# Optimization experiments

Measured on AMD Instinct MI355X. Metric: run time of the kernel, lower is better.

Reference implementation:

```python
import jax, jax.numpy as jnp
import numpy as np

N_NODES = 50000
N_EDGES = 800000
IN_CH, HID_CH, OUT_CH = 128, 128, 64


def _glorot(key, out_c, in_c):
    lim = (6.0 / (in_c + out_c)) ** 0.5
    return jax.random.uniform(key, (out_c, in_c), jnp.float32, -lim, lim)


def setup_inputs() -> dict:
    key = jax.random.key(0)
    ks = jax.random.split(key, 12)
    x = jax.random.normal(ks[0], (N_NODES, IN_CH), jnp.float32)
    edge_index = jax.random.randint(ks[1], (2, N_EDGES), 0, N_NODES, dtype=jnp.int64)
    # 4 SAGEConv layers: 128->128, 128->128, 128->64, 64->64
    dims = [(IN_CH, HID_CH), (HID_CH, HID_CH), (HID_CH, OUT_CH), (OUT_CH, OUT_CH)]
    params = {}
    for i, (ci, co) in enumerate(dims, start=1):
        params[f"Wl{i}"] = _glorot(ks[2 * i], co, ci)          # neighbor (aggregated) transform
        params[f"bl{i}"] = jnp.zeros((co,), jnp.float32)
        params[f"Wr{i}"] = _glorot(ks[2 * i + 1], co, ci)      # root/self transform (no bias in PyG)
    return {"x": x, "edge_index": edge_index, **params}


def _sage_conv(x, src, dst, Wl, bl, Wr):
    # mean aggregation of source features at destination nodes
    msgs = x[src]                                                   # [E, C] gather
    summed = jax.ops.segment_sum(msgs, dst, num_segments=N_NODES)   # [N, C] scatter-add
    cnt = jax.ops.segment_sum(jnp.ones((src.shape[0], 1), x.dtype), dst, num_segments=N_NODES)
    mean = summed / jnp.maximum(cnt, 1.0)
    return mean @ Wl.T + bl + x @ Wr.T


def reference(x, edge_index, Wl1, bl1, Wr1, Wl2, bl2, Wr2, Wl3, bl3, Wr3, Wl4, bl4, Wr4):
    src, dst = edge_index[0], edge_index[1]
    # conv1 = GraphSAGE(in, hid, num_layers=2): relu between layers only
    h = jax.nn.relu(_sage_conv(x, src, dst, Wl1, bl1, Wr1))
    h = _sage_conv(h, src, dst, Wl2, bl2, Wr2)
    h = jax.nn.relu(h)  # model-level .relu()
    # conv2 = GraphSAGE(hid, out, num_layers=2)
    h = jax.nn.relu(_sage_conv(h, src, dst, Wl3, bl3, Wr3))
    h = _sage_conv(h, src, dst, Wl4, bl4, Wr4)
    return jax.nn.log_softmax(h, axis=1)
```

## Files before the change

kernel.cpp:

```cpp
#include <hip/hip_runtime.h>
#include <hip/hip_bf16.h>


typedef __attribute__((ext_vector_type(8))) short bf16x8;
typedef __attribute__((ext_vector_type(4))) float f32x4;

#define NB 128
#define BSHIFT 9
#define BCAP 12288
#define EPB 2048

__device__ __forceinline__ unsigned short f2bf(float f) {
    __hip_bfloat16 h = __float2bfloat16(f);
    return __builtin_bit_cast(unsigned short, h);
}
__device__ __forceinline__ float bflo(unsigned int u) {
    return __builtin_bit_cast(float, u << 16);
}
__device__ __forceinline__ float bfhi(unsigned int u) {
    return __builtin_bit_cast(float, u & 0xffff0000u);
}

__global__ __launch_bounds__(256) void f2bf_bulk(const float* __restrict__ in,
                                                 unsigned short* __restrict__ out,
                                                 int n4) {
    int i = blockIdx.x * 256 + threadIdx.x;
    if (i < n4) {
        float4 v = reinterpret_cast<const float4*>(in)[i];
        ushort4 o = {f2bf(v.x), f2bf(v.y), f2bf(v.z), f2bf(v.w)};
        reinterpret_cast<ushort4*>(out)[i] = o;
    }
}

__global__ void zero_ints(int* __restrict__ p, int n) {
    int i = blockIdx.x * blockDim.x + threadIdx.x;
    if (i < n) p[i] = 0;
}

__global__ __launch_bounds__(256) void partition_edges(
    const int* __restrict__ ei, int E,
    int* __restrict__ gcur, unsigned int* __restrict__ ppk)
{
    __shared__ int hist[NB];
    __shared__ int base[NB];
    const int tid = threadIdx.x;
    for (int i = tid; i < NB; i += 256) hist[i] = 0;
    __syncthreads();

    const int e0 = blockIdx.x * EPB;
    int bket[8], rank[8];
    unsigned int pk[8];
    #pragma unroll
    for (int k = 0; k < 8; ++k) {
        int e = e0 + k * 256 + tid;
        bket[k] = -1;
        if (e < E) {
            int d = ei[E + e], s = ei[e];
            int b = d >> BSHIFT;
            bket[k] = b;
            pk[k] = ((unsigned int)(d - (b << BSHIFT)) << 16) | (unsigned int)s;
            rank[k] = atomicAdd(&hist[b], 1);
        }
    }
    __syncthreads();
    for (int i = tid; i < NB; i += 256)
        base[i] = hist[i] ? atomicAdd(&gcur[i], hist[i]) : 0;
    __syncthreads();
    #pragma unroll
    for (int k = 0; k < 8; ++k) {
        if (bket[k] >= 0) {
            int off = base[bket[k]] + rank[k];
            if (off < BCAP)
                ppk[(size_t)bket[k] * BCAP + off] = pk[k];
        }
    }
}

__global__ __launch_bounds__(256) void count_part(
    const unsigned int* __restrict__ ppk, const int* __restrict__ gcur,
    int* __restrict__ cnt)
{
    const int b = blockIdx.y;
    const int n = min(gcur[b], BCAP);
    const int tid = threadIdx.x;
    #pragma unroll
    for (int k = 0; k < 8; ++k) {
        int idx = blockIdx.x * EPB + k * 256 + tid;
        if (idx < n) {
            unsigned int pk = ppk[(size_t)b * BCAP + idx];
            atomicAdd(&cnt[(b << BSHIFT) + (int)(pk >> 16)], 1);
        }
    }
}

__global__ void block_sums(const int* __restrict__ cnt, int* __restrict__ bsum, int N) {
    int i = blockIdx.x * 256 + threadIdx.x;
    int v = (i < N) ? cnt[i] : 0;
    #pragma unroll
    for (int off = 32; off; off >>= 1) v += __shfl_down(v, off);
    __shared__ int ws_[4];
    int lane = threadIdx.x & 63, wid = threadIdx.x >> 6;
    if (lane == 0) ws_[wid] = v;
    __syncthreads();
    if (threadIdx.x == 0) bsum[blockIdx.x] = ws_[0] + ws_[1] + ws_[2] + ws_[3];
}

__global__ void scan_bsums(int* __restrict__ bsum, int nb) {
    int tid = threadIdx.x;
    int v = (tid < nb) ? bsum[tid] : 0;
    int lane = tid & 63, wid = tid >> 6;
    int x = v;
    #pragma unroll
    for (int d = 1; d < 64; d <<= 1) {
        int t = __shfl_up(x, d);
        if (lane >= d) x += t;
    }
    __shared__ int wsum[4];
    if (lane == 63) wsum[wid] = x;
    __syncthreads();
    int add = 0;
    for (int w = 0; w < wid; ++w) add += wsum[w];
    int incl = x + add;
    if (tid < nb) bsum[tid] = incl - v;
}

__global__ void scan_final(const int* __restrict__ cnt, const int* __restrict__ bsum,
                           int* __restrict__ offs, int* __restrict__ cursor, int N) {
    int b = blockIdx.x, tid = threadIdx.x;
    int i = b * 256 + tid;
    int v = (i < N) ? cnt[i] : 0;
    int lane = tid & 63, wid = tid >> 6;
    int x = v;
    #pragma unroll
    for (int d = 1; d < 64; d <<= 1) {
        int t = __shfl_up(x, d);
        if (lane >= d) x += t;
    }
    __shared__ int wsum[4];
    if (lane == 63) wsum[wid] = x;
    __syncthreads();
    int add = bsum[b];
    for (int w = 0; w < wid; ++w) add += wsum[w];
    int excl = add + x - v;
    if (i < N) { offs[i] = excl; cursor[i] = excl; }
    if (i == N - 1) offs[N] = excl + v;
}

__global__ __launch_bounds__(256) void fill_part(
    const unsigned int* __restrict__ ppk, const int* __restrict__ gcur,
    int* __restrict__ cursor, int* __restrict__ srcs)
{
    const int b = blockIdx.y;
    const int n = min(gcur[b], BCAP);
    const int tid = threadIdx.x;
    #pragma unroll
    for (int k = 0; k < 8; ++k) {
        int idx = blockIdx.x * EPB + k * 256 + tid;
        if (idx < n) {
            unsigned int pk = ppk[(size_t)b * BCAP + idx];
            int d = (b << BSHIFT) + (int)(pk >> 16);
            int slot = atomicAdd(&cursor[d], 1);
            srcs[slot] = (int)(pk & 0xffffu);
        }
    }
}

template <int K, int Cout, int ZBF>
__global__ __launch_bounds__(256) void gemm_yz_mfma(
    const unsigned short* __restrict__ H,
    const float* __restrict__ Wl, const float* __restrict__ Wr,
    unsigned short* __restrict__ Y, unsigned short* __restrict__ Zb,
    float* __restrict__ Zf, int N)
{
    constexpr int BM = 128, BN = 128;
    constexpr int ROWH = K + 8;
    __shared__ unsigned short Hs[BM * ROWH];
    __shared__ unsigned short Ws[BN * ROWH];

    const int tid = threadIdx.x;
    const int bm = blockIdx.x * BM;
    const int bn = blockIdx.y * BN;

    constexpr int C8 = K / 8;
    constexpr int NCH = BM * C8;
    #pragma unroll
    for (int c = tid; c < NCH; c += 256) {
        int row = c / C8, k8 = (c % C8) * 8;
        int grow = bm + row;
        int4 v = {0, 0, 0, 0};
        if (grow < N) v = *reinterpret_cast<const int4*>(&H[(size_t)grow * K + k8]);
        *reinterpret_cast<int4*>(&Hs[row * ROWH + k8]) = v;
    }
    constexpr int C4 = K / 4;
    constexpr int NCW = BN * C4;
    #pragma unroll
    for (int c = tid; c < NCW; c += 256) {
        int row = c / C4, k4 = (c % C4) * 4;
        int gcol = bn + row;
        const float* wsrc = (gcol < Cout) ? (Wl + (size_t)gcol * K)
                                          : (Wr + (size_t)(gcol - Cout) * K);
        float4 v = *reinterpret_cast<const float4*>(wsrc + k4);
        ushort4 o = {f2bf(v.x), f2bf(v.y), f2bf(v.z), f2bf(v.w)};
        *reinterpret_cast<ushort4*>(&Ws[row * ROWH + k4]) = o;
    }
    __syncthreads();

    const int wid = tid >> 6, lane = tid & 63;
    const int wr = wid >> 1, wc = wid & 1;
    const int l15 = lane & 15, lhi = lane >> 4;

    f32x4 acc[4][4] = {};
    #pragma unroll
    for (int k0 = 0; k0 < K; k0 += 32) {
        const int colOff = k0 + lhi * 8;
        bf16x8 a[4], b[4];
        #pragma unroll
        for (int m = 0; m < 4; ++m)
            a[m] = *reinterpret_cast<const bf16x8*>(&Hs[(wr * 64 + m * 16 + l15) * ROWH + colOff]);
        #pragma unroll
        for (int n = 0; n < 4; ++n)
            b[n] = *reinterpret_cast<const bf16x8*>(&Ws[(wc * 64 + n * 16 + l15) * ROWH + colOff]);
        #pragma unroll
        for (int m = 0; m < 4; ++m)
            #pragma unroll
            for (int n = 0; n < 4; ++n)
                acc[m][n] = __builtin_amdgcn_mfma_f32_16x16x32_bf16(a[m], b[n], acc[m][n], 0, 0, 0);
    }

    #pragma unroll
    for (int m = 0; m < 4; ++m) {
        #pragma unroll
        for (int n = 0; n < 4; ++n) {
            int gcol = bn + wc * 64 + n * 16 + l15;
            #pragma unroll
            for (int j = 0; j < 4; ++j) {
                int grow = bm + wr * 64 + m * 16 + lhi * 4 + j;
                if (grow < N) {
                    if (gcol < Cout)      Y[(size_t)grow * Cout + gcol] = f2bf(acc[m][n][j]);
                    else if (ZBF)         Zb[(size_t)grow * Cout + (gcol - Cout)] = f2bf(acc[m][n][j]);
                    else                  Zf[(size_t)grow * Cout + (gcol - Cout)] = acc[m][n][j];
                }
            }
        }
    }
}

__global__ __launch_bounds__(64) void agg128_bf(
    const unsigned short* __restrict__ Y, const unsigned short* __restrict__ Zb,
    const float* __restrict__ bl,
    const int* __restrict__ offs, const int* __restrict__ srcs,
    unsigned short* __restrict__ OUT)
{
    const int node = blockIdx.x;
    const int lane = threadIdx.x;
    const int beg = offs[node], end = offs[node + 1];

    float a0 = 0.f, a1 = 0.f;
    int e = beg;
    for (; e + 4 <= end; e += 4) {
        int s0 = srcs[e], s1 = srcs[e + 1], s2 = srcs[e + 2], s3 = srcs[e + 3];
        unsigned int u0 = *reinterpret_cast<const unsigned int*>(&Y[(size_t)s0 * 128 + 2 * lane]);
        unsigned int u1 = *reinterpret_cast<const unsigned int*>(&Y[(size_t)s1 * 128 + 2 * lane]);
        unsigned int u2 = *reinterpret_cast<const unsigned int*>(&Y[(size_t)s2 * 128 + 2 * lane]);
        unsigned int u3 = *reinterpret_cast<const unsigned int*>(&Y[(size_t)s3 * 128 + 2 * lane]);
        a0 += bflo(u0) + bflo(u1) + bflo(u2) + bflo(u3);
        a1 += bfhi(u0) + bfhi(u1) + bfhi(u2) + bfhi(u3);
    }
    for (; e < end; ++e) {
        unsigned int u = *reinterpret_cast<const unsigned int*>(&Y[(size_t)srcs[e] * 128 + 2 * lane]);
        a0 += bflo(u); a1 += bfhi(u);
    }
    float inv = 1.0f / fmaxf((float)(end - beg), 1.0f);
    unsigned int zu = *reinterpret_cast<const unsigned int*>(&Zb[(size_t)node * 128 + 2 * lane]);
    float2 bb = *reinterpret_cast<const float2*>(&bl[2 * lane]);
    float o0 = fmaxf(a0 * inv + bflo(zu) + bb.x, 0.f);
    float o1 = fmaxf(a1 * inv + bfhi(zu) + bb.y, 0.f);
    unsigned int packed = (unsigned int)f2bf(o0) | ((unsigned int)f2bf(o1) << 16);
    *reinterpret_cast<unsigned int*>(&OUT[(size_t)node * 128 + 2 * lane]) = packed;
}

template <int RELU, int BF16OUT, int ZBF>
__global__ __launch_bounds__(64) void agg64_k(
    const unsigned short* __restrict__ Y,
    const unsigned short* __restrict__ Zb, const float* __restrict__ Zf,
    const float* __restrict__ bl,
    const int* __restrict__ offs, const int* __restrict__ srcs,
    unsigned short* __restrict__ OUTb, float* __restrict__ OUTf)
{
    const int node = blockIdx.x;
    const int lane = threadIdx.x;
    const int half = lane >> 5, l31 = lane & 31;
    const int beg = offs[node], end = offs[node + 1];

    float a0 = 0.f, a1 = 0.f;
    int e = beg + half;
    for (; e + 2 < end; e += 4) {
        int s0 = srcs[e], s1 = srcs[e + 2];
        unsigned int u0 = *reinterpret_cast<const unsigned int*>(&Y[(size_t)s0 * 64 + 2 * l31]);
        unsigned int u1 = *reinterpret_cast<const unsigned int*>(&Y[(size_t)s1 * 64 + 2 * l31]);
        a0 += bflo(u0) + bflo(u1);
        a1 += bfhi(u0) + bfhi(u1);
    }
    if (e < end) {
        unsigned int u = *reinterpret_cast<const unsigned int*>(&Y[(size_t)srcs[e] * 64 + 2 * l31]);
        a0 += bflo(u); a1 += bfhi(u);
    }
    a0 += __shfl_xor(a0, 32);
    a1 += __shfl_xor(a1, 32);

    if (lane < 32) {
        float inv = 1.0f / fmaxf((float)(end - beg), 1.0f);
        float z0, z1;
        if (ZBF) {
            unsigned int zu = *reinterpret_cast<const unsigned int*>(&Zb[(size_t)node * 64 + 2 * l31]);
            z0 = bflo(zu); z1 = bfhi(zu);
        } else {
            float2 z = *reinterpret_cast<const float2*>(&Zf[(size_t)node * 64 + 2 * l31]);
            z0 = z.x; z1 = z.y;
        }
        float2 bb = *reinterpret_cast<const float2*>(&bl[2 * l31]);
        float o0 = a0 * inv + z0 + bb.x;
        float o1 = a1 * inv + z1 + bb.y;
        if (RELU) { o0 = fmaxf(o0, 0.f); o1 = fmaxf(o1, 0.f); }
        if (BF16OUT) {
            unsigned int packed = (unsigned int)f2bf(o0) | ((unsigned int)f2bf(o1) << 16);
            *reinterpret_cast<unsigned int*>(&OUTb[(size_t)node * 64 + 2 * l31]) = packed;
        } else {
            *reinterpret_cast<float2*>(&OUTf[(size_t)node * 64 + 2 * l31]) = make_float2(o0, o1);
        }
    }
}

__global__ __launch_bounds__(64) void logsoftmax64(
    const float* __restrict__ in, float* __restrict__ out, int N)
{
    const int r = blockIdx.x;
    const int lane = threadIdx.x;
    float v = in[(size_t)r * 64 + lane];
    float m = v;
    #pragma unroll
    for (int off = 32; off; off >>= 1) m = fmaxf(m, __shfl_xor(m, off));
    float e = expf(v - m);
    float s = e;
    #pragma unroll
    for (int off = 32; off; off >>= 1) s += __shfl_xor(s, off);
    out[(size_t)r * 64 + lane] = (v - m) - logf(s);
}

extern "C" void kernel_launch(void* const* d_in, const int* in_sizes, int n_in,
                              void* d_out, int out_size, void* d_ws, size_t ws_size,
                              hipStream_t stream) {
    const float* x   = (const float*)d_in[0];
    const int*   ei  = (const int*)d_in[1];
    const float* Wl1 = (const float*)d_in[2];
    const float* bl1 = (const float*)d_in[3];
    const float* Wr1 = (const float*)d_in[4];
    const float* Wl2 = (const float*)d_in[5];
    const float* bl2 = (const float*)d_in[6];
    const float* Wr2 = (const float*)d_in[7];
    const float* Wl3 = (const float*)d_in[8];
    const float* bl3 = (const float*)d_in[9];
    const float* Wr3 = (const float*)d_in[10];
    const float* Wl4 = (const float*)d_in[11];
    const float* bl4 = (const float*)d_in[12];
    const float* Wr4 = (const float*)d_in[13];

    const int N = in_sizes[0] / 128;
    const int E = in_sizes[1] / 2;

    char* p = (char*)d_ws;
    auto alloc = [&](size_t bytes) {
        char* r = p;
        p += (bytes + 255) & ~(size_t)255;
        return r;
    };
    int*            cnt    = (int*)alloc((size_t)N * 4);
    int*            offs   = (int*)alloc((size_t)(N + 1) * 4);
    int*            cursor = (int*)alloc((size_t)N * 4);
    int*            bsum   = (int*)alloc(256 * 4);
    int*            gcur   = (int*)alloc(NB * 4);
    unsigned int*   ppk    = (unsigned int*)alloc((size_t)NB * BCAP * 4);
    int*            srcs   = (int*)alloc((size_t)E * 4);
    unsigned short* xb     = (unsigned short*)alloc((size_t)N * 128 * 2);
    unsigned short* ybuf   = (unsigned short*)alloc((size_t)N * 128 * 2);
    char*           zraw   = alloc((size_t)N * 128 * 4);
    unsigned short* h1     = (unsigned short*)alloc((size_t)N * 128 * 2);
    unsigned short* h2     = (unsigned short*)alloc((size_t)N * 128 * 2);
    unsigned short* h3     = (unsigned short*)alloc((size_t)N * 64 * 2);
    float*          hf     = (float*)alloc((size_t)N * 64 * 4);
    unsigned short* zb     = (unsigned short*)zraw;
    float*          zf     = (float*)zraw;
    (void)ws_size; (void)n_in; (void)out_size;

    const int nb = (N + 255) / 256;
    const int mtiles = (N + 127) / 128;

    f2bf_bulk<<<(N * 128 / 4 + 255) / 256, 256, 0, stream>>>(x, xb, N * 128 / 4);

    zero_ints<<<(N + 255) / 256, 256, 0, stream>>>(cnt, N);
    zero_ints<<<1, NB, 0, stream>>>(gcur, NB);
    partition_edges<<<(E + EPB - 1) / EPB, 256, 0, stream>>>(ei, E, gcur, ppk);
    count_part<<<dim3(BCAP / EPB, NB), 256, 0, stream>>>(ppk, gcur, cnt);
    block_sums<<<nb, 256, 0, stream>>>(cnt, bsum, N);
    scan_bsums<<<1, 256, 0, stream>>>(bsum, nb);
    scan_final<<<nb, 256, 0, stream>>>(cnt, bsum, offs, cursor, N);
    fill_part<<<dim3(BCAP / EPB, NB), 256, 0, stream>>>(ppk, gcur, cursor, srcs);

    gemm_yz_mfma<128, 128, 1><<<dim3(mtiles, 2), 256, 0, stream>>>(xb, Wl1, Wr1, ybuf, zb, nullptr, N);
    agg128_bf<<<N, 64, 0, stream>>>(ybuf, zb, bl1, offs, srcs, h1);
    gemm_yz_mfma<128, 128, 1><<<dim3(mtiles, 2), 256, 0, stream>>>(h1, Wl2, Wr2, ybuf, zb, nullptr, N);
    agg128_bf<<<N, 64, 0, stream>>>(ybuf, zb, bl2, offs, srcs, h2);
    gemm_yz_mfma<128, 64, 1><<<dim3(mtiles, 1), 256, 0, stream>>>(h2, Wl3, Wr3, ybuf, zb, nullptr, N);
    agg64_k<1, 1, 1><<<N, 64, 0, stream>>>(ybuf, zb, nullptr, bl3, offs, srcs, h3, nullptr);
    gemm_yz_mfma<64, 64, 0><<<dim3(mtiles, 1), 256, 0, stream>>>(h3, Wl4, Wr4, ybuf, nullptr, zf, N);
    agg64_k<0, 0, 0><<<N, 64, 0, stream>>>(ybuf, nullptr, zf, bl4, offs, srcs, nullptr, hf);

    logsoftmax64<<<N, 64, 0, stream>>>(hf, (float*)d_out, N);
}
```

Before: 374.7 us.

## Replace CSR build with per-bucket LDS sort and fuse conversion and log-softmax

The multi-kernel CSR build (count, three-stage scan, fill with global atomics) is replaced by finer 512-bucket partitioning, a single-block scan of bucket totals, and a per-bucket shared-memory counting sort that writes srcs and offs directly. The standalone fp32-to-bf16 conversion of x is folded into the first GEMM's tile load, and log-softmax is fused into the last aggregation kernel. Aggregation kernels now pack four nodes per 256-thread block. This cuts kernel launches, global atomics and intermediate buffers. It relies on every bucket holding at most 3072 edges and on per-bucket ordering being consistent.

```diff
diff --git a/kernel.cpp b/kernel.cpp
--- a/kernel.cpp
+++ b/kernel.cpp
@@ -5,9 +5,9 @@
 typedef __attribute__((ext_vector_type(8))) short bf16x8;
 typedef __attribute__((ext_vector_type(4))) float f32x4;
 
-#define NB 128
-#define BSHIFT 9
-#define BCAP 12288
+#define NBKT 512
+#define BSHIFT 7
+#define BCAP 3072
 #define EPB 2048
 
 __device__ __forceinline__ unsigned short f2bf(float f) {
@@ -21,17 +21,6 @@
     return __builtin_bit_cast(float, u & 0xffff0000u);
 }
 
-__global__ __launch_bounds__(256) void f2bf_bulk(const float* __restrict__ in,
-                                                 unsigned short* __restrict__ out,
-                                                 int n4) {
-    int i = blockIdx.x * 256 + threadIdx.x;
-    if (i < n4) {
-        float4 v = reinterpret_cast<const float4*>(in)[i];
-        ushort4 o = {f2bf(v.x), f2bf(v.y), f2bf(v.z), f2bf(v.w)};
-        reinterpret_cast<ushort4*>(out)[i] = o;
-    }
-}
-
 __global__ void zero_ints(int* __restrict__ p, int n) {
     int i = blockIdx.x * blockDim.x + threadIdx.x;
     if (i < n) p[i] = 0;
@@ -41,10 +30,10 @@
     const int* __restrict__ ei, int E,
     int* __restrict__ gcur, unsigned int* __restrict__ ppk)
 {
-    __shared__ int hist[NB];
-    __shared__ int base[NB];
+    __shared__ int hist[NBKT];
+    __shared__ int base[NBKT];
     const int tid = threadIdx.x;
-    for (int i = tid; i < NB; i += 256) hist[i] = 0;
+    for (int i = tid; i < NBKT; i += 256) hist[i] = 0;
     __syncthreads();
 
     const int e0 = blockIdx.x * EPB;
@@ -58,12 +47,12 @@
             int d = ei[E + e], s = ei[e];
             int b = d >> BSHIFT;
             bket[k] = b;
-            pk[k] = ((unsigned int)(d - (b << BSHIFT)) << 16) | (unsigned int)s;
+            pk[k] = ((unsigned int)(d & ((1 << BSHIFT) - 1)) << 16) | (unsigned int)s;
             rank[k] = atomicAdd(&hist[b], 1);
         }
     }
     __syncthreads();
-    for (int i = tid; i < NB; i += 256)
+    for (int i = tid; i < NBKT; i += 256)
         base[i] = hist[i] ? atomicAdd(&gcur[i], hist[i]) : 0;
     __syncthreads();
     #pragma unroll
@@ -76,98 +65,82 @@
     }
 }
 
-__global__ __launch_bounds__(256) void count_part(
-    const unsigned int* __restrict__ ppk, const int* __restrict__ gcur,
-    int* __restrict__ cnt)
-{
-    const int b = blockIdx.y;
-    const int n = min(gcur[b], BCAP);
+__global__ __launch_bounds__(512) void scan_gcur(
+    const int* __restrict__ gcur, int* __restrict__ bbase,
+    int* __restrict__ offs, int N)
+{
     const int tid = threadIdx.x;
-    #pragma unroll
-    for (int k = 0; k < 8; ++k) {
-        int idx = blockIdx.x * EPB + k * 256 + tid;
-        if (idx < n) {
-            unsigned int pk = ppk[(size_t)b * BCAP + idx];
-            atomicAdd(&cnt[(b << BSHIFT) + (int)(pk >> 16)], 1);
-        }
-    }
-}
-
-__global__ void block_sums(const int* __restrict__ cnt, int* __restrict__ bsum, int N) {
-    int i = blockIdx.x * 256 + threadIdx.x;
-    int v = (i < N) ? cnt[i] : 0;
-    #pragma unroll
-    for (int off = 32; off; off >>= 1) v += __shfl_down(v, off);
-    __shared__ int ws_[4];
-    int lane = threadIdx.x & 63, wid = threadIdx.x >> 6;
-    if (lane == 0) ws_[wid] = v;
-    __syncthreads();
-    if (threadIdx.x == 0) bsum[blockIdx.x] = ws_[0] + ws_[1] + ws_[2] + ws_[3];
-}
-
-__global__ void scan_bsums(int* __restrict__ bsum, int nb) {
-    int tid = threadIdx.x;
-    int v = (tid < nb) ? bsum[tid] : 0;
-    int lane = tid & 63, wid = tid >> 6;
+    int v = min(gcur[tid], BCAP);
     int x = v;
     #pragma unroll
     for (int d = 1; d < 64; d <<= 1) {
         int t = __shfl_up(x, d);
-        if (lane >= d) x += t;
-    }
-    __shared__ int wsum[4];
-    if (lane == 63) wsum[wid] = x;
+        if ((tid & 63) >= d) x += t;
+    }
+    __shared__ int ws[8];
+    if ((tid & 63) == 63) ws[tid >> 6] = x;
     __syncthreads();
     int add = 0;
-    for (int w = 0; w < wid; ++w) add += wsum[w];
+    for (int w = 0; w < (tid >> 6); ++w) add += ws[w];
     int incl = x + add;
-    if (tid < nb) bsum[tid] = incl - v;
-}
-
-__global__ void scan_final(const int* __restrict__ cnt, const int* __restrict__ bsum,
-                           int* __restrict__ offs, int* __restrict__ cursor, int N) {
-    int b = blockIdx.x, tid = threadIdx.x;
-    int i = b * 256 + tid;
-    int v = (i < N) ? cnt[i] : 0;
-    int lane = tid & 63, wid = tid >> 6;
-    int x = v;
-    #pragma unroll
-    for (int d = 1; d < 64; d <<= 1) {
-        int t = __shfl_up(x, d);
-        if (lane >= d) x += t;
-    }
-    __shared__ int wsum[4];
-    if (lane == 63) wsum[wid] = x;
-    __syncthreads();
-    int add = bsum[b];
-    for (int w = 0; w < wid; ++w) add += wsum[w];
-    int excl = add + x - v;
-    if (i < N) { offs[i] = excl; cursor[i] = excl; }
-    if (i == N - 1) offs[N] = excl + v;
-}
-
-__global__ __launch_bounds__(256) void fill_part(
+    bbase[tid] = incl - v;
+    if (tid == 511) offs[N] = incl;
+}
+
+__global__ __launch_bounds__(256) void bucket_sort(
     const unsigned int* __restrict__ ppk, const int* __restrict__ gcur,
-    int* __restrict__ cursor, int* __restrict__ srcs)
-{
-    const int b = blockIdx.y;
+    const int* __restrict__ bbase,
+    int* __restrict__ offs, int* __restrict__ srcs, int N)
+{
+    const int b = blockIdx.x;
     const int n = min(gcur[b], BCAP);
+    const int bb = bbase[b];
     const int tid = threadIdx.x;
-    #pragma unroll
-    for (int k = 0; k < 8; ++k) {
-        int idx = blockIdx.x * EPB + k * 256 + tid;
-        if (idx < n) {
-            unsigned int pk = ppk[(size_t)b * BCAP + idx];
-            int d = (b << BSHIFT) + (int)(pk >> 16);
-            int slot = atomicAdd(&cursor[d], 1);
-            srcs[slot] = (int)(pk & 0xffffu);
-        }
-    }
-}
-
-template <int K, int Cout, int ZBF>
+
+    __shared__ unsigned int eL[BCAP];
+    __shared__ int cnt[1 << BSHIFT], excl[1 << BSHIFT], cur[1 << BSHIFT];
+
+    if (tid < (1 << BSHIFT)) cnt[tid] = 0;
+    for (int i = tid; i < n; i += 256) eL[i] = ppk[(size_t)b * BCAP + i];
+    __syncthreads();
+    for (int i = tid; i < n; i += 256) atomicAdd(&cnt[eL[i] >> 16], 1);
+    __syncthreads();
+
+    int v = 0, x = 0;
+    if (tid < 128) {
+        v = cnt[tid];
+        x = v;
+        #pragma unroll
+        for (int d = 1; d < 64; d <<= 1) {
+            int t = __shfl_up(x, d);
+            if ((tid & 63) >= d) x += t;
+        }
+    }
+    __shared__ int w0;
+    if (tid == 63) w0 = x;
+    __syncthreads();
+    if (tid < 128) {
+        int incl = x + ((tid >= 64) ? w0 : 0);
+        excl[tid] = incl - v;
+        cur[tid] = incl - v;
+    }
+    __syncthreads();
+
+    for (int i = tid; i < n; i += 256) {
+        unsigned int pk = eL[i];
+        int d = (int)(pk >> 16);
+        int pos = atomicAdd(&cur[d], 1);
+        srcs[bb + pos] = (int)(pk & 0xffffu);
+    }
+    if (tid < 128) {
+        int gn = (b << BSHIFT) + tid;
+        if (gn < N) offs[gn] = bb + excl[tid];
+    }
+}
+
+template <int K, int Cout, int ZBF, int F32IN>
 __global__ __launch_bounds__(256) void gemm_yz_mfma(
-    const unsigned short* __restrict__ H,
+    const void* __restrict__ Hv,
     const float* __restrict__ Wl, const float* __restrict__ Wr,
     unsigned short* __restrict__ Y, unsigned short* __restrict__ Zb,
     float* __restrict__ Zf, int N)
@@ -181,27 +154,39 @@
     const int bm = blockIdx.x * BM;
     const int bn = blockIdx.y * BN;
 
-    constexpr int C8 = K / 8;
-    constexpr int NCH = BM * C8;
-    #pragma unroll
-    for (int c = tid; c < NCH; c += 256) {
-        int row = c / C8, k8 = (c % C8) * 8;
-        int grow = bm + row;
-        int4 v = {0, 0, 0, 0};
-        if (grow < N) v = *reinterpret_cast<const int4*>(&H[(size_t)grow * K + k8]);
-        *reinterpret_cast<int4*>(&Hs[row * ROWH + k8]) = v;
-    }
-    constexpr int C4 = K / 4;
-    constexpr int NCW = BN * C4;
-    #pragma unroll
-    for (int c = tid; c < NCW; c += 256) {
-        int row = c / C4, k4 = (c % C4) * 4;
-        int gcol = bn + row;
-        const float* wsrc = (gcol < Cout) ? (Wl + (size_t)gcol * K)
-                                          : (Wr + (size_t)(gcol - Cout) * K);
-        float4 v = *reinterpret_cast<const float4*>(wsrc + k4);
-        ushort4 o = {f2bf(v.x), f2bf(v.y), f2bf(v.z), f2bf(v.w)};
-        *reinterpret_cast<ushort4*>(&Ws[row * ROWH + k4]) = o;
+    if (F32IN) {
+        const float* H = (const float*)Hv;
+        constexpr int C4 = K / 4;
+        for (int c = tid; c < BM * C4; c += 256) {
+            int row = c / C4, k4 = (c % C4) * 4;
+            int grow = bm + row;
+            float4 vv = make_float4(0.f, 0.f, 0.f, 0.f);
+            if (grow < N) vv = *reinterpret_cast<const float4*>(&H[(size_t)grow * K + k4]);
+            ushort4 o = {f2bf(vv.x), f2bf(vv.y), f2bf(vv.z), f2bf(vv.w)};
+            *reinterpret_cast<ushort4*>(&Hs[row * ROWH + k4]) = o;
+        }
+    } else {
+        const unsigned short* H = (const unsigned short*)Hv;
+        constexpr int C8 = K / 8;
+        for (int c = tid; c < BM * C8; c += 256) {
+            int row = c / C8, k8 = (c % C8) * 8;
+            int grow = bm + row;
+            int4 vv = {0, 0, 0, 0};
+            if (grow < N) vv = *reinterpret_cast<const int4*>(&H[(size_t)grow * K + k8]);
+            *reinterpret_cast<int4*>(&Hs[row * ROWH + k8]) = vv;
+        }
+    }
+    {
+        constexpr int C4 = K / 4;
+        for (int c = tid; c < BN * C4; c += 256) {
+            int row = c / C4, k4 = (c % C4) * 4;
+            int gcol = bn + row;
+            const float* wsrc = (gcol < Cout) ? (Wl + (size_t)gcol * K)
+                                              : (Wr + (size_t)(gcol - Cout) * K);
+            float4 vv = *reinterpret_cast<const float4*>(wsrc + k4);
+            ushort4 o = {f2bf(vv.x), f2bf(vv.y), f2bf(vv.z), f2bf(vv.w)};
+            *reinterpret_cast<ushort4*>(&Ws[row * ROWH + k4]) = o;
+        }
     }
     __syncthreads();
 
@@ -213,46 +198,47 @@
     #pragma unroll
     for (int k0 = 0; k0 < K; k0 += 32) {
         const int colOff = k0 + lhi * 8;
-        bf16x8 a[4], b[4];
+        bf16x8 a[4], bfr[4];
         #pragma unroll
         for (int m = 0; m < 4; ++m)
             a[m] = *reinterpret_cast<const bf16x8*>(&Hs[(wr * 64 + m * 16 + l15) * ROWH + colOff]);
         #pragma unroll
-        for (int n = 0; n < 4; ++n)
-            b[n] = *reinterpret_cast<const bf16x8*>(&Ws[(wc * 64 + n * 16 + l15) * ROWH + colOff]);
+        for (int nn = 0; nn < 4; ++nn)
+            bfr[nn] = *reinterpret_cast<const bf16x8*>(&Ws[(wc * 64 + nn * 16 + l15) * ROWH + colOff]);
         #pragma unroll
         for (int m = 0; m < 4; ++m)
             #pragma unroll
-            for (int n = 0; n < 4; ++n)
-                acc[m][n] = __builtin_amdgcn_mfma_f32_16x16x32_bf16(a[m], b[n], acc[m][n], 0, 0, 0);
+            for (int nn = 0; nn < 4; ++nn)
+                acc[m][nn] = __builtin_amdgcn_mfma_f32_16x16x32_bf16(a[m], bfr[nn], acc[m][nn], 0, 0, 0);
     }
 
     #pragma unroll
     for (int m = 0; m < 4; ++m) {
         #pragma unroll
-        for (int n = 0; n < 4; ++n) {
-            int gcol = bn + wc * 64 + n * 16 + l15;
+        for (int nn = 0; nn < 4; ++nn) {
+            int gcol = bn + wc * 64 + nn * 16 + l15;
             #pragma unroll
             for (int j = 0; j < 4; ++j) {
                 int grow = bm + wr * 64 + m * 16 + lhi * 4 + j;
                 if (grow < N) {
-                    if (gcol < Cout)      Y[(size_t)grow * Cout + gcol] = f2bf(acc[m][n][j]);
-                    else if (ZBF)         Zb[(size_t)grow * Cout + (gcol - Cout)] = f2bf(acc[m][n][j]);
-                    else                  Zf[(size_t)grow * Cout + (gcol - Cout)] = acc[m][n][j];
+                    if (gcol < Cout)      Y[(size_t)grow * Cout + gcol] = f2bf(acc[m][nn][j]);
+                    else if (ZBF)         Zb[(size_t)grow * Cout + (gcol - Cout)] = f2bf(acc[m][nn][j]);
+                    else                  Zf[(size_t)grow * Cout + (gcol - Cout)] = acc[m][nn][j];
                 }
             }
         }
     }
 }
 
-__global__ __launch_bounds__(64) void agg128_bf(
+__global__ __launch_bounds__(256) void agg128_bf(
     const unsigned short* __restrict__ Y, const unsigned short* __restrict__ Zb,
     const float* __restrict__ bl,
     const int* __restrict__ offs, const int* __restrict__ srcs,
-    unsigned short* __restrict__ OUT)
-{
-    const int node = blockIdx.x;
-    const int lane = threadIdx.x;
+    unsigned short* __restrict__ OUT, int N)
+{
+    const int node = blockIdx.x * 4 + (threadIdx.x >> 6);
+    if (node >= N) return;
+    const int lane = threadIdx.x & 63;
     const int beg = offs[node], end = offs[node + 1];
 
     float a0 = 0.f, a1 = 0.f;
@@ -279,16 +265,15 @@
     *reinterpret_cast<unsigned int*>(&OUT[(size_t)node * 128 + 2 * lane]) = packed;
 }
 
-template <int RELU, int BF16OUT, int ZBF>
-__global__ __launch_bounds__(64) void agg64_k(
-    const unsigned short* __restrict__ Y,
-    const unsigned short* __restrict__ Zb, const float* __restrict__ Zf,
+__global__ __launch_bounds__(256) void agg64_mid(
+    const unsigned short* __restrict__ Y, const unsigned short* __restrict__ Zb,
     const float* __restrict__ bl,
     const int* __restrict__ offs, const int* __restrict__ srcs,
-    unsigned short* __restrict__ OUTb, float* __restrict__ OUTf)
-{
-    const int node = blockIdx.x;
-    const int lane = threadIdx.x;
+    unsigned short* __restrict__ OUT, int N)
+{
+    const int node = blockIdx.x * 4 + (threadIdx.x >> 6);
+    if (node >= N) return;
+    const int lane = threadIdx.x & 63;
     const int half = lane >> 5, l31 = lane & 31;
     const int beg = offs[node], end = offs[node + 1];
 
@@ -308,43 +293,61 @@
     a0 += __shfl_xor(a0, 32);
     a1 += __shfl_xor(a1, 32);
 
-    if (lane < 32) {
+    if (half == 0) {
         float inv = 1.0f / fmaxf((float)(end - beg), 1.0f);
-        float z0, z1;
-        if (ZBF) {
-            unsigned int zu = *reinterpret_cast<const unsigned int*>(&Zb[(size_t)node * 64 + 2 * l31]);
-            z0 = bflo(zu); z1 = bfhi(zu);
-        } else {
-            float2 z = *reinterpret_cast<const float2*>(&Zf[(size_t)node * 64 + 2 * l31]);
-            z0 = z.x; z1 = z.y;
-        }
+        unsigned int zu = *reinterpret_cast<const unsigned int*>(&Zb[(size_t)node * 64 + 2 * l31]);
         float2 bb = *reinterpret_cast<const float2*>(&bl[2 * l31]);
-        float o0 = a0 * inv + z0 + bb.x;
-        float o1 = a1 * inv + z1 + bb.y;
-        if (RELU) { o0 = fmaxf(o0, 0.f); o1 = fmaxf(o1, 0.f); }
-        if (BF16OUT) {
-            unsigned int packed = (unsigned int)f2bf(o0) | ((unsigned int)f2bf(o1) << 16);
-            *reinterpret_cast<unsigned int*>(&OUTb[(size_t)node * 64 + 2 * l31]) = packed;
-        } else {
-            *reinterpret_cast<float2*>(&OUTf[(size_t)node * 64 + 2 * l31]) = make_float2(o0, o1);
-        }
-    }
-}
-
-__global__ __launch_bounds__(64) void logsoftmax64(
-    const float* __restrict__ in, float* __restrict__ out, int N)
-{
-    const int r = blockIdx.x;
-    const int lane = threadIdx.x;
-    float v = in[(size_t)r * 64 + lane];
-    float m = v;
-    #pragma unroll
-    for (int off = 32; off; off >>= 1) m = fmaxf(m, __shfl_xor(m, off));
-    float e = expf(v - m);
-    float s = e;
-    #pragma unroll
-    for (int off = 32; off; off >>= 1) s += __shfl_xor(s, off);
-    out[(size_t)r * 64 + lane] = (v - m) - logf(s);
+        float o0 = fmaxf(a0 * inv + bflo(zu) + bb.x, 0.f);
+        float o1 = fmaxf(a1 * inv + bfhi(zu) + bb.y, 0.f);
+        unsigned int packed = (unsigned int)f2bf(o0) | ((unsigned int)f2bf(o1) << 16);
+        *reinterpret_cast<unsigned int*>(&OUT[(size_t)node * 64 + 2 * l31]) = packed;
+    }
+}
+
+__global__ __launch_bounds__(256) void agg64_lsm(
+    const unsigned short* __restrict__ Y, const float* __restrict__ Zf,
+    const float* __restrict__ bl,
+    const int* __restrict__ offs, const int* __restrict__ srcs,
+    float* __restrict__ OUT, int N)
+{
+    const int node = blockIdx.x * 4 + (threadIdx.x >> 6);
+    if (node >= N) return;
+    const int lane = threadIdx.x & 63;
+    const int half = lane >> 5, l31 = lane & 31;
+    const int beg = offs[node], end = offs[node + 1];
+
+    float a0 = 0.f, a1 = 0.f;
+    int e = beg + half;
+    for (; e + 2 < end; e += 4) {
+        int s0 = srcs[e], s1 = srcs[e + 2];
+        unsigned int u0 = *reinterpret_cast<const unsigned int*>(&Y[(size_t)s0 * 64 + 2 * l31]);
+        unsigned int u1 = *reinterpret_cast<const unsigned int*>(&Y[(size_t)s1 * 64 + 2 * l31]);
+        a0 += bflo(u0) + bflo(u1);
+        a1 += bfhi(u0) + bfhi(u1);
+    }
+    if (e < end) {
+        unsigned int u = *reinterpret_cast<const unsigned int*>(&Y[(size_t)srcs[e] * 64 + 2 * l31]);
+        a0 += bflo(u); a1 += bfhi(u);
+    }
+    a0 += __shfl_xor(a0, 32);
+    a1 += __shfl_xor(a1, 32);
+
+    float inv = 1.0f / fmaxf((float)(end - beg), 1.0f);
+    float2 z = *reinterpret_cast<const float2*>(&Zf[(size_t)node * 64 + 2 * l31]);
+    float2 bb = *reinterpret_cast<const float2*>(&bl[2 * l31]);
+    float o0 = a0 * inv + z.x + bb.x;
+    float o1 = a1 * inv + z.y + bb.y;
+
+    float m = fmaxf(o0, o1);
+    #pragma unroll
+    for (int off = 16; off; off >>= 1) m = fmaxf(m, __shfl_xor(m, off));
+    float s = expf(o0 - m) + expf(o1 - m);
+    #pragma unroll
+    for (int off = 16; off; off >>= 1) s += __shfl_xor(s, off);
+    float ls = logf(s);
+    if (half == 0)
+        *reinterpret_cast<float2*>(&OUT[(size_t)node * 64 + 2 * l31]) =
+            make_float2(o0 - m - ls, o1 - m - ls);
 }
 
 extern "C" void kernel_launch(void* const* d_in, const int* in_sizes, int n_in,
@@ -374,46 +377,35 @@
         p += (bytes + 255) & ~(size_t)255;
         return r;
     };
-    int*            cnt    = (int*)alloc((size_t)N * 4);
-    int*            offs   = (int*)alloc((size_t)(N + 1) * 4);
-    int*            cursor = (int*)alloc((size_t)N * 4);
-    int*            bsum   = (int*)alloc(256 * 4);
-    int*            gcur   = (int*)alloc(NB * 4);
-    unsigned int*   ppk    = (unsigned int*)alloc((size_t)NB * BCAP * 4);
-    int*            srcs   = (int*)alloc((size_t)E * 4);
-    unsigned short* xb     = (unsigned short*)alloc((size_t)N * 128 * 2);
-    unsigned short* ybuf   = (unsigned short*)alloc((size_t)N * 128 * 2);
-    char*           zraw   = alloc((size_t)N * 128 * 4);
-    unsigned short* h1     = (unsigned short*)alloc((size_t)N * 128 * 2);
-    unsigned short* h2     = (unsigned short*)alloc((size_t)N * 128 * 2);
-    unsigned short* h3     = (unsigned short*)alloc((size_t)N * 64 * 2);
-    float*          hf     = (float*)alloc((size_t)N * 64 * 4);
-    unsigned short* zb     = (unsigned short*)zraw;
-    float*          zf     = (float*)zraw;
+    int*            offs  = (int*)alloc((size_t)(N + 1) * 4);
+    int*            gcur  = (int*)alloc(NBKT * 4);
+    int*            bbase = (int*)alloc(NBKT * 4);
+    unsigned int*   ppk   = (unsigned int*)alloc((size_t)NBKT * BCAP * 4);
+    int*            srcs  = (int*)alloc((size_t)E * 4);
+    unsigned short* ybuf  = (unsigned short*)alloc((size_t)N * 128 * 2);
+    char*           zraw  = alloc((size_t)N * 128 * 4);
+    unsigned short* h1    = (unsigned short*)alloc((size_t)N * 128 * 2);
+    unsigned short* h2    = (unsigned short*)alloc((size_t)N * 128 * 2);
+    unsigned short* h3    = (unsigned short*)alloc((size_t)N * 64 * 2);
+    unsigned short* zb    = (unsigned short*)zraw;
+    float*          zf    = (float*)zraw;
     (void)ws_size; (void)n_in; (void)out_size;
 
-    const int nb = (N + 255) / 256;
     const int mtiles = (N + 127) / 128;
-
-    f2bf_bulk<<<(N * 128 / 4 + 255) / 256, 256, 0, stream>>>(x, xb, N * 128 / 4);
-
-    zero_ints<<<(N + 255) / 256, 256, 0, stream>>>(cnt, N);
-    zero_ints<<<1, NB, 0, stream>>>(gcur, NB);
+    const int nbkt_used = (N + (1 << BSHIFT) - 1) >> BSHIFT;
+    const int aggblocks = (N + 3) / 4;
+
+    zero_ints<<<1, NBKT, 0, stream>>>(gcur, NBKT);
     partition_edges<<<(E + EPB - 1) / EPB, 256, 0, stream>>>(ei, E, gcur, ppk);
-    count_part<<<dim3(BCAP / EPB, NB), 256, 0, stream>>>(ppk, gcur, cnt);
-    block_sums<<<nb, 256, 0, stream>>>(cnt, bsum, N);
-    scan_bsums<<<1, 256, 0, stream>>>(bsum, nb);
-    scan_final<<<nb, 256, 0, stream>>>(cnt, bsum, offs, cursor, N);
-    fill_part<<<dim3(BCAP / EPB, NB), 256, 0, stream>>>(ppk, gcur, cursor, srcs);
-
-    gemm_yz_mfma<128, 128, 1><<<dim3(mtiles, 2), 256, 0, stream>>>(xb, Wl1, Wr1, ybuf, zb, nullptr, N);
-    agg128_bf<<<N, 64, 0, stream>>>(ybuf, zb, bl1, offs, srcs, h1);
-    gemm_yz_mfma<128, 128, 1><<<dim3(mtiles, 2), 256, 0, stream>>>(h1, Wl2, Wr2, ybuf, zb, nullptr, N);
-    agg128_bf<<<N, 64, 0, stream>>>(ybuf, zb, bl2, offs, srcs, h2);
-    gemm_yz_mfma<128, 64, 1><<<dim3(mtiles, 1), 256, 0, stream>>>(h2, Wl3, Wr3, ybuf, zb, nullptr, N);
-    agg64_k<1, 1, 1><<<N, 64, 0, stream>>>(ybuf, zb, nullptr, bl3, offs, srcs, h3, nullptr);
-    gemm_yz_mfma<64, 64, 0><<<dim3(mtiles, 1), 256, 0, stream>>>(h3, Wl4, Wr4, ybuf, nullptr, zf, N);
-    agg64_k<0, 0, 0><<<N, 64, 0, stream>>>(ybuf, nullptr, zf, bl4, offs, srcs, nullptr, hf);
-
-    logsoftmax64<<<N, 64, 0, stream>>>(hf, (float*)d_out, N);
-}
+    scan_gcur<<<1, NBKT, 0, stream>>>(gcur, bbase, offs, N);
+    bucket_sort<<<nbkt_used, 256, 0, stream>>>(ppk, gcur, bbase, offs, srcs, N);
+
+    gemm_yz_mfma<128, 128, 1, 1><<<dim3(mtiles, 2), 256, 0, stream>>>(x, Wl1, Wr1, ybuf, zb, nullptr, N);
+    agg128_bf<<<aggblocks, 256, 0, stream>>>(ybuf, zb, bl1, offs, srcs, h1, N);
+    gemm_yz_mfma<128, 128, 1, 0><<<dim3(mtiles, 2), 256, 0, stream>>>(h1, Wl2, Wr2, ybuf, zb, nullptr, N);
+    agg128_bf<<<aggblocks, 256, 0, stream>>>(ybuf, zb, bl2, offs, srcs, h2, N);
+    gemm_yz_mfma<128, 64, 1, 0><<<dim3(mtiles, 1), 256, 0, stream>>>(h2, Wl3, Wr3, ybuf, zb, nullptr, N);
+    agg64_mid<<<aggblocks, 256, 0, stream>>>(ybuf, zb, bl3, offs, srcs, h3, N);
+    gemm_yz_mfma<64, 64, 0, 0><<<dim3(mtiles, 1), 256, 0, stream>>>(h3, Wl4, Wr4, ybuf, nullptr, zf, N);
+    agg64_lsm<<<aggblocks, 256, 0, stream>>>(ybuf, zf, bl4, offs, srcs, (float*)d_out, N);
+}
```

New measurement: 349.6 us. 1.07x faster.
